# Optimization experiments

Hardware: AMD Instinct MI355X
Metric: run time of the kernel (lower is better)

## Reference

```python
import jax, jax.numpy as jnp
import numpy as np

# Segmented tensor product, uniform-1d case (subscripts 'u,u,u'):
#   out[z, idx_out[p]*u:(idx_out[p]+1)*u] += coeffs[p] * x0_seg[z, idx0[p]] * x1_seg[z, idx1[p]]
U = 128          # mode extent 'u'
NSEG = (32, 8, 32)  # segments per operand (in0, in1, out)
P = 128          # number of paths
Z = 16384        # batch


def setup_inputs() -> dict:
    key = jax.random.key(0)
    k0, k1, k2, k3, k4, k5 = jax.random.split(key, 6)
    return {
        "x0": jax.random.normal(k0, (Z, NSEG[0] * U), dtype=jnp.float32),
        "x1": jax.random.normal(k1, (Z, NSEG[1] * U), dtype=jnp.float32),
        "coeffs": jax.random.normal(k2, (P,), dtype=jnp.float32),
        "idx0": jax.random.randint(k3, (P,), 0, NSEG[0], dtype=jnp.int32),
        "idx1": jax.random.randint(k4, (P,), 0, NSEG[1], dtype=jnp.int32),
        "idx_out": jax.random.randint(k5, (P,), 0, NSEG[2], dtype=jnp.int32),
    }


def reference(x0, x1, coeffs, idx0, idx1, idx_out):
    z = x0.shape[0]
    x0r = x0.reshape(z, NSEG[0], U)  # [Z, n0, u]
    x1r = x1.reshape(z, NSEG[1], U)  # [Z, n1, u]
    # gather the segment used by each path: [Z, P, u]
    s0 = x0r[:, idx0, :]
    s1 = x1r[:, idx1, :]
    # per-path contribution, elementwise over u (coefficient subscript is scalar)
    contrib = (s0 * s1) * coeffs[None, :, None]          # [Z, P, u]
    # scatter-add paths into output segments
    contrib = jnp.transpose(contrib, (1, 0, 2))          # [P, Z, u]
    out_seg = jax.ops.segment_sum(contrib, idx_out, num_segments=NSEG[2])  # [n2, Z, u]
    return jnp.transpose(out_seg, (1, 0, 2)).reshape(z, NSEG[2] * U)
```

## Files before the change

kernel.cpp:

```cpp
#include <hip/hip_runtime.h>


#define Z_DIM 16384
#define U_DIM 128
#define NSEG0 32
#define NSEG1 8
#define NSEG2 32
#define P_DIM 128
#define ZPB   2
#define BLK   512

__global__ __launch_bounds__(BLK) void tp_kernel(
    const float* __restrict__ x0,
    const float* __restrict__ x1,
    const float* __restrict__ coeffs,
    const int* __restrict__ idx0,
    const int* __restrict__ idx1,
    const int* __restrict__ idx_out,
    float* __restrict__ out)
{
    __shared__ float s_x0[ZPB][NSEG0 * U_DIM];
    __shared__ float s_x1[ZPB][NSEG1 * U_DIM];
    __shared__ int2  s_meta[P_DIM];
    __shared__ int   s_cnt[NSEG2];
    __shared__ int   s_off[NSEG2];

    const int t = threadIdx.x;

    int my_o = 0, my_i0 = 0, my_i1 = 0, my_cb = 0;
    if (t < P_DIM) {
        my_o  = idx_out[t];
        my_i0 = idx0[t];
        my_i1 = idx1[t];
        my_cb = __float_as_int(coeffs[t]);
    }
    if (t < NSEG2) s_cnt[t] = 0;

    {
        const size_t z0 = (size_t)blockIdx.x * ZPB;
        const float4* g0 = reinterpret_cast<const float4*>(x0 + z0 * (NSEG0 * U_DIM));
        const float4* g1 = reinterpret_cast<const float4*>(x1 + z0 * (NSEG1 * U_DIM));
        float4* l0 = reinterpret_cast<float4*>(&s_x0[0][0]);
        float4* l1 = reinterpret_cast<float4*>(&s_x1[0][0]);
        #pragma unroll
        for (int i = 0; i < (ZPB * NSEG0 * U_DIM / 4) / BLK; ++i)
            l0[i * BLK + t] = g0[i * BLK + t];
        #pragma unroll
        for (int i = 0; i < (ZPB * NSEG1 * U_DIM / 4) / BLK; ++i)
            l1[i * BLK + t] = g1[i * BLK + t];
    }
    __syncthreads();

    int my_rank = 0;
    if (t < P_DIM) my_rank = atomicAdd(&s_cnt[my_o], 1);
    __syncthreads();
    if (t < NSEG2) {
        int sum = 0;
        for (int o = 0; o < t; ++o) sum += s_cnt[o];
        s_off[t] = sum;
    }
    __syncthreads();
    if (t < P_DIM)
        s_meta[s_off[my_o] + my_rank] = make_int2(my_i0 | (my_i1 << 16), my_cb);
    __syncthreads();

    const int wave = t >> 6;
    const int zl   = (t >> 5) & 1;
    const int uq   = t & 31;

    const float* x0base = &s_x0[zl][uq * 4];
    const float* x1base = &s_x1[zl][uq * 4];
    const size_t z = (size_t)blockIdx.x * ZPB + zl;
    float4* orow = reinterpret_cast<float4*>(out + z * (NSEG2 * U_DIM)) + uq;

    #pragma unroll
    for (int oo = 0; oo < 4; ++oo) {
        const int o = wave * 4 + oo;
        const int b = s_off[o];
        const int e = b + s_cnt[o];
        float4 acc = make_float4(0.f, 0.f, 0.f, 0.f);
        for (int k = b; k < e; ++k) {
            const int2  m = s_meta[k];
            const float c = __int_as_float(m.y);
            const float4 a = *reinterpret_cast<const float4*>(x0base + (m.x & 0xffff) * U_DIM);
            const float4 v = *reinterpret_cast<const float4*>(x1base + (m.x >> 16)    * U_DIM);
            acc.x = fmaf(c, a.x * v.x, acc.x);
            acc.y = fmaf(c, a.y * v.y, acc.y);
            acc.z = fmaf(c, a.z * v.z, acc.z);
            acc.w = fmaf(c, a.w * v.w, acc.w);
        }
        orow[o * (U_DIM / 4)] = acc;
    }
}

extern "C" void kernel_launch(void* const* d_in, const int* in_sizes, int n_in,
                              void* d_out, int out_size, void* d_ws, size_t ws_size,
                              hipStream_t stream) {
    const float* x0      = (const float*)d_in[0];
    const float* x1      = (const float*)d_in[1];
    const float* coeffs  = (const float*)d_in[2];
    const int*   idx0    = (const int*)d_in[3];
    const int*   idx1    = (const int*)d_in[4];
    const int*   idx_out = (const int*)d_in[5];
    float* out = (float*)d_out;

    const int blocks = Z_DIM / ZPB;
    tp_kernel<<<blocks, BLK, 0, stream>>>(x0, x1, coeffs, idx0, idx1, idx_out, out);
}
```

Before: 114.1 us.

## Hoist path bucketing into setup kernel and use direct global-to-LDS loads

Moves the per-block counting sort of paths by output segment into a single-block setup kernel that writes offsets and packed metadata to workspace. The main kernel then reads these through uniform global loads, which removes three block barriers and the shared atomics from every block. It also stages x0 and x1 into LDS with global_load_lds when the builtin exists, skipping the round trip through registers. In exchange it adds a second kernel launch and a dependency between the two launches.

Result: slower. 118.0 us (+3.4%).

```diff
diff --git a/kernel.cpp b/kernel.cpp
--- a/kernel.cpp
+++ b/kernel.cpp
@@ -10,77 +10,87 @@
 #define ZPB   2
 #define BLK   512
 
-__global__ __launch_bounds__(BLK) void tp_kernel(
-    const float* __restrict__ x0,
-    const float* __restrict__ x1,
+__global__ __launch_bounds__(128) void tp_setup(
     const float* __restrict__ coeffs,
     const int* __restrict__ idx0,
     const int* __restrict__ idx1,
     const int* __restrict__ idx_out,
+    int* __restrict__ off_g,
+    int2* __restrict__ meta_g)
+{
+    __shared__ int s_cnt[NSEG2];
+    __shared__ int s_off[NSEG2 + 1];
+    const int t = threadIdx.x;
+    if (t < NSEG2) s_cnt[t] = 0;
+    __syncthreads();
+    const int o = idx_out[t];
+    const int r = atomicAdd(&s_cnt[o], 1);
+    __syncthreads();
+    if (t == 0) {
+        int sum = 0;
+        for (int i = 0; i < NSEG2; ++i) { s_off[i] = sum; sum += s_cnt[i]; }
+        s_off[NSEG2] = sum;
+    }
+    __syncthreads();
+    meta_g[s_off[o] + r] = make_int2(idx0[t] | (idx1[t] << 16), __float_as_int(coeffs[t]));
+    if (t <= NSEG2) off_g[t] = s_off[t];
+}
+
+__global__ __launch_bounds__(BLK) void tp_kernel(
+    const float* __restrict__ x0,
+    const float* __restrict__ x1,
+    const int* __restrict__ off_g,
+    const int2* __restrict__ meta_g,
     float* __restrict__ out)
 {
     __shared__ float s_x0[ZPB][NSEG0 * U_DIM];
     __shared__ float s_x1[ZPB][NSEG1 * U_DIM];
-    __shared__ int2  s_meta[P_DIM];
-    __shared__ int   s_cnt[NSEG2];
-    __shared__ int   s_off[NSEG2];
 
     const int t = threadIdx.x;
-
-    int my_o = 0, my_i0 = 0, my_i1 = 0, my_cb = 0;
-    if (t < P_DIM) {
-        my_o  = idx_out[t];
-        my_i0 = idx0[t];
-        my_i1 = idx1[t];
-        my_cb = __float_as_int(coeffs[t]);
-    }
-    if (t < NSEG2) s_cnt[t] = 0;
+    const size_t z0 = (size_t)blockIdx.x * ZPB;
 
     {
-        const size_t z0 = (size_t)blockIdx.x * ZPB;
         const float4* g0 = reinterpret_cast<const float4*>(x0 + z0 * (NSEG0 * U_DIM));
         const float4* g1 = reinterpret_cast<const float4*>(x1 + z0 * (NSEG1 * U_DIM));
         float4* l0 = reinterpret_cast<float4*>(&s_x0[0][0]);
         float4* l1 = reinterpret_cast<float4*>(&s_x1[0][0]);
+#if __has_builtin(__builtin_amdgcn_global_load_lds)
+        #pragma unroll
+        for (int i = 0; i < (ZPB * NSEG0 * U_DIM / 4) / BLK; ++i)
+            __builtin_amdgcn_global_load_lds(
+                (const __attribute__((address_space(1))) void*)(g0 + i * BLK + t),
+                (__attribute__((address_space(3))) void*)(l0 + i * BLK + t),
+                16, 0, 0);
+        __builtin_amdgcn_global_load_lds(
+            (const __attribute__((address_space(1))) void*)(g1 + t),
+            (__attribute__((address_space(3))) void*)(l1 + t),
+            16, 0, 0);
+#else
         #pragma unroll
         for (int i = 0; i < (ZPB * NSEG0 * U_DIM / 4) / BLK; ++i)
             l0[i * BLK + t] = g0[i * BLK + t];
-        #pragma unroll
-        for (int i = 0; i < (ZPB * NSEG1 * U_DIM / 4) / BLK; ++i)
-            l1[i * BLK + t] = g1[i * BLK + t];
+        l1[t] = g1[t];
+#endif
     }
     __syncthreads();
 
-    int my_rank = 0;
-    if (t < P_DIM) my_rank = atomicAdd(&s_cnt[my_o], 1);
-    __syncthreads();
-    if (t < NSEG2) {
-        int sum = 0;
-        for (int o = 0; o < t; ++o) sum += s_cnt[o];
-        s_off[t] = sum;
-    }
-    __syncthreads();
-    if (t < P_DIM)
-        s_meta[s_off[my_o] + my_rank] = make_int2(my_i0 | (my_i1 << 16), my_cb);
-    __syncthreads();
-
-    const int wave = t >> 6;
-    const int zl   = (t >> 5) & 1;
-    const int uq   = t & 31;
+    const int w4 = __builtin_amdgcn_readfirstlane(t >> 6) * 4;
+    const int zl = (t >> 5) & 1;
+    const int uq = t & 31;
 
     const float* x0base = &s_x0[zl][uq * 4];
     const float* x1base = &s_x1[zl][uq * 4];
-    const size_t z = (size_t)blockIdx.x * ZPB + zl;
+    const size_t z = z0 + zl;
     float4* orow = reinterpret_cast<float4*>(out + z * (NSEG2 * U_DIM)) + uq;
 
     #pragma unroll
     for (int oo = 0; oo < 4; ++oo) {
-        const int o = wave * 4 + oo;
-        const int b = s_off[o];
-        const int e = b + s_cnt[o];
+        const int o = w4 + oo;
+        const int b = off_g[o];
+        const int e = off_g[o + 1];
         float4 acc = make_float4(0.f, 0.f, 0.f, 0.f);
         for (int k = b; k < e; ++k) {
-            const int2  m = s_meta[k];
+            const int2  m = meta_g[k];
             const float c = __int_as_float(m.y);
             const float4 a = *reinterpret_cast<const float4*>(x0base + (m.x & 0xffff) * U_DIM);
             const float4 v = *reinterpret_cast<const float4*>(x1base + (m.x >> 16)    * U_DIM);
@@ -104,6 +114,9 @@
     const int*   idx_out = (const int*)d_in[5];
     float* out = (float*)d_out;
 
-    const int blocks = Z_DIM / ZPB;
-    tp_kernel<<<blocks, BLK, 0, stream>>>(x0, x1, coeffs, idx0, idx1, idx_out, out);
+    int*  off_g  = (int*)d_ws;
+    int2* meta_g = (int2*)((char*)d_ws + 256);
+
+    tp_setup<<<1, P_DIM, 0, stream>>>(coeffs, idx0, idx1, idx_out, off_g, meta_g);
+    tp_kernel<<<Z_DIM / ZPB, BLK, 0, stream>>>(x0, x1, off_g, meta_g, out);
 }
```
